# Kernel tuning notes

Hardware: AMD Instinct MI355X
Metric: run time of the kernel (lower is better)

The kernel has to match this reference:

```python
import jax, jax.numpy as jnp
import numpy as np

HIDDEN = 512
BATCH = 64
SEQ = 1024


def setup_inputs() -> dict:
    key = jax.random.key(0)
    ks = jax.random.split(key, 16)
    H = HIDDEN
    s = 0.05
    inp = {
        'x': jax.random.normal(ks[0], (BATCH, SEQ), dtype=jnp.float32),
        # layer 1: input size 1
        'W_ih1': jax.random.normal(ks[1], (4 * H, 1), dtype=jnp.float32) * s,
        'W_hh1': jax.random.normal(ks[2], (4 * H, H), dtype=jnp.float32) * s,
        'b_ih1': jax.random.normal(ks[3], (4 * H,), dtype=jnp.float32) * s,
        'b_hh1': jax.random.normal(ks[4], (4 * H,), dtype=jnp.float32) * s,
        # layer 2
        'W_ih2': jax.random.normal(ks[5], (4 * H, H), dtype=jnp.float32) * s,
        'W_hh2': jax.random.normal(ks[6], (4 * H, H), dtype=jnp.float32) * s,
        'b_ih2': jax.random.normal(ks[7], (4 * H,), dtype=jnp.float32) * s,
        'b_hh2': jax.random.normal(ks[8], (4 * H,), dtype=jnp.float32) * s,
        # layer 3
        'W_ih3': jax.random.normal(ks[9], (4 * H, H), dtype=jnp.float32) * s,
        'W_hh3': jax.random.normal(ks[10], (4 * H, H), dtype=jnp.float32) * s,
        'b_ih3': jax.random.normal(ks[11], (4 * H,), dtype=jnp.float32) * s,
        'b_hh3': jax.random.normal(ks[12], (4 * H,), dtype=jnp.float32) * s,
        # output projection
        'W_lin': jax.random.normal(ks[13], (1, H), dtype=jnp.float32) * s,
        'b_lin': jax.random.normal(ks[14], (1,), dtype=jnp.float32) * s,
    }
    return inp


def _lstm_cell(x, h, c, W_ih, W_hh, b_ih, b_hh):
    # PyTorch LSTMCell: gates ordered [i, f, g, o]
    gates = x @ W_ih.T + b_ih + h @ W_hh.T + b_hh  # [B, 4H]
    i, f, g, o = jnp.split(gates, 4, axis=-1)
    i = jax.nn.sigmoid(i)
    f = jax.nn.sigmoid(f)
    g = jnp.tanh(g)
    o = jax.nn.sigmoid(o)
    c_new = f * c + i * g
    h_new = o * jnp.tanh(c_new)
    return h_new, c_new


def reference(x, W_ih1, W_hh1, b_ih1, b_hh1,
              W_ih2, W_hh2, b_ih2, b_hh2,
              W_ih3, W_hh3, b_ih3, b_hh3,
              W_lin, b_lin):
    B = x.shape[0]
    H = W_hh1.shape[1]
    z = jnp.zeros((B, H), dtype=x.dtype)
    init = (z, z, z, z, z, z)  # h1,c1,h2,c2,h3,c3

    def step(carry, x_t):
        h1, c1, h2, c2, h3, c3 = carry
        h1, c1 = _lstm_cell(x_t, h1, c1, W_ih1, W_hh1, b_ih1, b_hh1)
        h2, c2 = _lstm_cell(h1, h2, c2, W_ih2, W_hh2, b_ih2, b_hh2)
        h3, c3 = _lstm_cell(h2, h3, c3, W_ih3, W_hh3, b_ih3, b_hh3)
        out = h3 @ W_lin.T + b_lin  # [B, 1]
        return (h1, c1, h2, c2, h3, c3), out

    xs = x.T[:, :, None]  # [T, B, 1]
    _, outs = jax.lax.scan(step, init, xs)  # outs: [T, B, 1]
    return outs[:, :, 0].T  # [B, T]
```

## Files before the change

kernel.cpp:

```cpp
#include <hip/hip_runtime.h>
#include <cstdint>
#include <cstddef>


typedef __attribute__((ext_vector_type(8))) short bf16x8;
typedef __attribute__((ext_vector_type(4))) float f32x4;
typedef __attribute__((ext_vector_type(2))) unsigned long long u64x2;

#define TT    1024
#define RINGD 8
#define NBL   64
#define NGRID (3*NBL + 1)
#define SENT  0xFFFFFFFFu

#define OFF_W1   0ULL
#define OFF_W2   (OFF_W1 + 2048ULL*512*2)
#define OFF_W3   (OFF_W2 + 2048ULL*1024*2)
#define OFF_BIAS (OFF_W3 + 2048ULL*1024*2)
#define OFF_FLAG (OFF_BIAS + 3ULL*2048*4)
#define OFF_RING (OFF_FLAG + 4096ULL)
#define NEED_BIG (OFF_RING + 3ULL*TT*64*512*2)

__device__ __forceinline__ unsigned short f2bf(float f) {
  unsigned int u = __float_as_uint(f);
  unsigned int r = (u + 0x7fffu + ((u >> 16) & 1u)) >> 16;
  return (unsigned short)r;
}
__device__ __forceinline__ float bf2f(unsigned short h) {
  return __uint_as_float(((unsigned int)h) << 16);
}
__device__ __forceinline__ float sigmf_(float z) {
  return 1.f / (1.f + __expf(-z));
}
__device__ __forceinline__ float tanhf_(float z) {
  float t = __expf(-2.f * fabsf(z));
  float r = (1.f - t) / (1.f + t);
  return (z < 0.f) ? -r : r;
}

__global__ void prep_kernel(const float* __restrict__ wih1, const float* __restrict__ whh1,
                            const float* __restrict__ bih1, const float* __restrict__ bhh1,
                            const float* __restrict__ wih2, const float* __restrict__ whh2,
                            const float* __restrict__ bih2, const float* __restrict__ bhh2,
                            const float* __restrict__ wih3, const float* __restrict__ whh3,
                            const float* __restrict__ bih3, const float* __restrict__ bhh3,
                            unsigned char* ws, int big)
{
  unsigned short* w1 = (unsigned short*)(ws + OFF_W1);
  unsigned short* w2 = (unsigned short*)(ws + OFF_W2);
  unsigned short* w3 = (unsigned short*)(ws + OFF_W3);
  float* bias = (float*)(ws + OFF_BIAS);
  int*   flags = (int*)(ws + OFF_FLAG);
  int idx = blockIdx.x * 256 + threadIdx.x;
  int j = idx >> 10, k = idx & 1023;
  if (j < 2048) {
    float v2 = (k < 512) ? wih2[j*512 + k] : whh2[j*512 + (k - 512)];
    float v3 = (k < 512) ? wih3[j*512 + k] : whh3[j*512 + (k - 512)];
    w2[j*1024 + k] = f2bf(v2);
    w3[j*1024 + k] = f2bf(v3);
    if (k < 512) w1[j*512 + k] = f2bf(whh1[j*512 + k]);
  }
  if (idx < 2048) {
    bias[idx]        = bih1[idx] + bhh1[idx];
    bias[2048 + idx] = bih2[idx] + bhh2[idx];
    bias[4096 + idx] = bih3[idx] + bhh3[idx];
  }
  if (idx < 256) flags[idx] = 0;
  if (big) {
    uint4* r4 = (uint4*)(ws + OFF_RING);
    uint4 s; s.x = SENT; s.y = SENT; s.z = SENT; s.w = SENT;
    for (size_t i = idx; i < 12582912ULL; i += 2097152ULL) r4[i] = s;
  }
}

template<int KSTEPS>
__device__ __forceinline__ void compute_tiles(const bf16x8 (&warr)[32], const char* smemc,
                                              int wv, int ln15, int kgrp,
                                              f32x4 (&acc)[2][4])
{
  const int k0w = wv * (KSTEPS * 32);
  const int sw  = (ln15 & 7) << 4;
  #pragma unroll
  for (int s = 0; s < KSTEPS; ++s) {
    const int koff = k0w + s*32 + kgrp*8;
    const int r    = koff >> 9;
    const int kin  = koff & 511;
    const char* ab = smemc + r*32768;
    bf16x8 a0 = *(const bf16x8*)(ab + ((ln15*1024        + kin*2) ^ sw));
    bf16x8 a1 = *(const bf16x8*)(ab + (((ln15 + 16)*1024 + kin*2) ^ sw));
    #pragma unroll
    for (int gt = 0; gt < 4; ++gt) {
      acc[0][gt] = __builtin_amdgcn_mfma_f32_16x16x32_bf16(a0, warr[gt*KSTEPS + s], acc[0][gt], 0, 0, 0);
      acc[1][gt] = __builtin_amdgcn_mfma_f32_16x16x32_bf16(a1, warr[gt*KSTEPS + s], acc[1][gt], 0, 0, 0);
    }
  }
}

__global__ __launch_bounds__(256, 1) void rnn_kernel(
    unsigned char* ws, const float* __restrict__ x,
    const float* __restrict__ wih1, const float* __restrict__ wlin,
    const float* __restrict__ blin, float* __restrict__ out, int big)
{
  __shared__ __align__(128) char smem[65536];
  const int tid  = threadIdx.x;
  const int lane = tid & 63;
  const int wv   = tid >> 6;
  const int SLOTS = big ? TT : RINGD;
  int* flags = (int*)(ws + OFF_FLAG);
  unsigned int* ringw = (unsigned int*)(ws + OFF_RING);
  const unsigned long long* ringq = (const unsigned long long*)(ws + OFF_RING);

  if (blockIdx.x == NGRID - 1) {
    float* wl = (float*)smem;
    float* op = (float*)(smem + 4096);
    if (tid < 128) ((f32x4*)wl)[tid] = ((const f32x4*)wlin)[tid];
    float blv = blin[0];
    __syncthreads();
    const int ob = tid >> 2, okq = tid & 3;
    const int* fup = flags + 2*64 + lane;
    for (int t = 0; t < TT; ++t) {
      if (!big && wv == 0) {
        for (;;) {
          int v = __hip_atomic_load(fup, __ATOMIC_RELAXED, __HIP_MEMORY_SCOPE_AGENT);
          if (__all(v >= t + 1)) break;
          __builtin_amdgcn_s_sleep(2);
        }
      }
      asm volatile("" ::: "memory");
      __syncthreads();
      const int slot = big ? t : (t & 7);
      size_t ebase = ((size_t)(2*SLOTS + slot) * 64 + ob) * 512 + (size_t)okq * 128;
      const unsigned long long* hp = ringq + (ebase >> 2);
      const float* wlp = wl + okq * 128;
      unsigned long long qv[32];
      if (big) {
        #pragma unroll
        for (int i = 0; i < 32; ++i) qv[i] = hp[i];
        for (;;) {
          int bad = 0;
          #pragma unroll
          for (int i = 0; i < 32; ++i)
            bad |= ((unsigned int)qv[i] == SENT) | ((unsigned int)(qv[i] >> 32) == SENT);
          if (!bad) break;
          __builtin_amdgcn_s_sleep(2);
          #pragma unroll
          for (int i = 0; i < 32; ++i)
            qv[i] = __hip_atomic_load(hp + i, __ATOMIC_RELAXED, __HIP_MEMORY_SCOPE_AGENT);
        }
      } else {
        #pragma unroll
        for (int i = 0; i < 32; ++i)
          qv[i] = __hip_atomic_load(hp + i, __ATOMIC_RELAXED, __HIP_MEMORY_SCOPE_AGENT);
      }
      float acc = 0.f;
      #pragma unroll
      for (int i = 0; i < 32; ++i) {
        acc += bf2f((unsigned short)(qv[i]      )) * wlp[i*4 + 0];
        acc += bf2f((unsigned short)(qv[i] >> 16)) * wlp[i*4 + 1];
        acc += bf2f((unsigned short)(qv[i] >> 32)) * wlp[i*4 + 2];
        acc += bf2f((unsigned short)(qv[i] >> 48)) * wlp[i*4 + 3];
      }
      op[ob*4 + okq] = acc;
      __syncthreads();
      if (tid < 64)
        out[(size_t)tid * TT + t] = op[tid*4] + op[tid*4+1] + op[tid*4+2] + op[tid*4+3] + blv;
      if (!big && tid == 0)
        __hip_atomic_store(flags + 3*64, t + 1, __ATOMIC_RELEASE, __HIP_MEMORY_SCOPE_AGENT);
      __syncthreads();
    }
    return;
  }

  const int g  = blockIdx.x >> 6;
  const int q  = blockIdx.x & 63;
  const int bh = q & 1;
  const int nbase = (q >> 1) << 4;
  const unsigned short* Wg =
      (const unsigned short*)(ws + (g == 0 ? OFF_W1 : (g == 1 ? OFF_W2 : OFF_W3)));
  const float* biasg = (const float*)(ws + OFF_BIAS) + g * 2048;

  const int ln15 = lane & 15;
  const int kgrp = lane >> 4;

  bf16x8 warr[32];
  if (g == 0) {
    #pragma unroll
    for (int gt = 0; gt < 4; ++gt)
      #pragma unroll
      for (int s = 0; s < 4; ++s)
        warr[gt*4 + s] = *(const bf16x8*)(Wg + (size_t)(gt*512 + nbase + ln15)*512
                                             + wv*128 + s*32 + kgrp*8);
  } else {
    #pragma unroll
    for (int gt = 0; gt < 4; ++gt)
      #pragma unroll
      for (int s = 0; s < 8; ++s)
        warr[gt*8 + s] = *(const bf16x8*)(Wg + (size_t)(gt*512 + nbase + ln15)*1024
                                             + wv*256 + s*32 + kgrp*8);
  }

  const int eb  = tid >> 3;
  const int n0  = (tid & 7) << 1;
  const int bge = bh * 32 + eb;
  float bsv[4][2], wxv[4][2];
  #pragma unroll
  for (int gt = 0; gt < 4; ++gt) {
    #pragma unroll
    for (int cc = 0; cc < 2; ++cc) {
      int jj = gt*512 + nbase + n0 + cc;
      bsv[gt][cc] = biasg[jj];
      wxv[gt][cc] = (g == 0) ? wih1[jj] : 0.f;
    }
  }
  float cst0 = 0.f, cst1 = 0.f;

  const int l31 = lane & 31;
  int* myflag = flags + g*64 + q;
  const int* fup  = flags + (g > 0 ? (g - 1)*64 : 0) + 2*l31 + bh;
  const int* fsib = flags + g*64 + 2*l31 + bh;
  const int* fdn  = (g < 2) ? (flags + (g + 1)*64 + 2*l31 + bh) : (flags + 3*64);

  const int sbi = tid >> 3, skc = tid & 7;
  const int swz = (sbi & 7) << 4;

  auto stage_big = [&](int gg, int tick, int r) {
    size_t ebase = ((size_t)(gg*TT + tick) * 64 + bh*32 + sbi) * 512;
    const unsigned long long* src = ringq + (ebase >> 2);
    char* dst = smem + r*32768 + sbi*1024;
    unsigned long long v[16];
    #pragma unroll
    for (int i = 0; i < 8; ++i) {
      v[2*i]   = src[(i*8 + skc)*2];
      v[2*i+1] = src[(i*8 + skc)*2 + 1];
    }
    for (;;) {
      int bad = 0;
      #pragma unroll
      for (int i = 0; i < 16; ++i)
        bad |= ((unsigned int)v[i] == SENT) | ((unsigned int)(v[i] >> 32) == SENT);
      if (!bad) break;
      __builtin_amdgcn_s_sleep(2);
      #pragma unroll
      for (int i = 0; i < 8; ++i) {
        v[2*i]   = __hip_atomic_load(src + (i*8 + skc)*2,     __ATOMIC_RELAXED, __HIP_MEMORY_SCOPE_AGENT);
        v[2*i+1] = __hip_atomic_load(src + (i*8 + skc)*2 + 1, __ATOMIC_RELAXED, __HIP_MEMORY_SCOPE_AGENT);
      }
    }
    #pragma unroll
    for (int i = 0; i < 8; ++i) {
      u64x2 w; w[0] = v[2*i]; w[1] = v[2*i+1];
      *(u64x2*)(dst + (((i*8 + skc) * 16) ^ swz)) = w;
    }
  };
  auto stage_small = [&](int gg, int slot, int r) {
    size_t ebase = ((size_t)(gg*RINGD + slot) * 64 + bh*32 + sbi) * 512;
    const unsigned long long* src = ringq + (ebase >> 2);
    char* dst = smem + r*32768 + sbi*1024;
    unsigned long long v[16];
    #pragma unroll
    for (int i = 0; i < 16; ++i)
      v[i] = __hip_atomic_load(src + (i*8 + skc), __ATOMIC_RELAXED, __HIP_MEMORY_SCOPE_AGENT);
    #pragma unroll
    for (int i = 0; i < 16; ++i)
      *(unsigned long long*)(dst + (((i*8 + skc) * 8) ^ swz)) = v[i];
  };
  auto zero_region = [&](int r) {
    char* dst = smem + r*32768 + sbi*1024;
    #pragma unroll
    for (int i = 0; i < 16; ++i)
      *(unsigned long long*)(dst + (((i*8 + skc) * 8) ^ swz)) = 0ULL;
  };

  if (g > 0) {
    if (big) {
      stage_big(g - 1, 0, 0);
    } else {
      if (wv == 0) {
        for (;;) {
          int v = __hip_atomic_load(fup, __ATOMIC_RELAXED, __HIP_MEMORY_SCOPE_AGENT);
          if (__all(v >= 1)) break;
          __builtin_amdgcn_s_sleep(2);
        }
      }
      asm volatile("" ::: "memory");
      __syncthreads();
      stage_small(g - 1, 0, 0);
    }
  }

  for (int t = 0; t < TT; ++t) {
    const int slot = big ? t : (t & 7);
    if (!big && wv == 0) {
      for (;;) {
        int ok = 1;
        if (t >= 1) {
          int v = __hip_atomic_load(fsib, __ATOMIC_RELAXED, __HIP_MEMORY_SCOPE_AGENT);
          ok &= (v >= t);
        }
        if (t >= RINGD) {
          int v = __hip_atomic_load(fdn, __ATOMIC_RELAXED, __HIP_MEMORY_SCOPE_AGENT);
          ok &= (v >= t - RINGD + 1);
        }
        if (__all(ok)) break;
        __builtin_amdgcn_s_sleep(2);
      }
    }
    asm volatile("" ::: "memory");
    __syncthreads();
    const int hr = (g == 0) ? 0 : 1;
    if (t == 0)       zero_region(hr);
    else if (big)     stage_big(g, t - 1, hr);
    else              stage_small(g, (t - 1) & 7, hr);
    __syncthreads();

    f32x4 acc[2][4];
    #pragma unroll
    for (int a = 0; a < 2; ++a) {
      #pragma unroll
      for (int b = 0; b < 4; ++b) { f32x4 z = {0.f, 0.f, 0.f, 0.f}; acc[a][b] = z; }
    }
    if (g == 0) compute_tiles<4>(warr, smem, wv, ln15, kgrp, acc);
    else        compute_tiles<8>(warr, smem, wv, ln15, kgrp, acc);
    __syncthreads();

    float* part = (float*)smem;
    #pragma unroll
    for (int bt = 0; bt < 2; ++bt) {
      #pragma unroll
      for (int gt = 0; gt < 4; ++gt) {
        #pragma unroll
        for (int rr = 0; rr < 4; ++rr) {
          int brow = bt*16 + kgrp*4 + rr;
          int jj   = gt*16 + ln15;
          part[(wv*32 + brow)*64 + (jj ^ ((brow & 3) << 4))] = acc[bt][gt][rr];
        }
      }
    }
    __syncthreads();

    float Gv[4][2];
    #pragma unroll
    for (int gt = 0; gt < 4; ++gt) {
      #pragma unroll
      for (int cc = 0; cc < 2; ++cc) {
        int jx = (gt*16 + n0 + cc) ^ ((eb & 3) << 4);
        Gv[gt][cc] = part[(0*32 + eb)*64 + jx] + part[(1*32 + eb)*64 + jx]
                   + part[(2*32 + eb)*64 + jx] + part[(3*32 + eb)*64 + jx]
                   + bsv[gt][cc];
      }
    }
    if (g == 0) {
      float xv = x[(size_t)bge * TT + t];
      #pragma unroll
      for (int gt = 0; gt < 4; ++gt) {
        Gv[gt][0] += xv * wxv[gt][0];
        Gv[gt][1] += xv * wxv[gt][1];
      }
    }
    float i0 = sigmf_(Gv[0][0]), f0 = sigmf_(Gv[1][0]), gA = tanhf_(Gv[2][0]), o0 = sigmf_(Gv[3][0]);
    float i1 = sigmf_(Gv[0][1]), f1 = sigmf_(Gv[1][1]), gB = tanhf_(Gv[2][1]), o1 = sigmf_(Gv[3][1]);
    cst0 = f0 * cst0 + i0 * gA;
    cst1 = f1 * cst1 + i1 * gB;
    float h0 = o0 * tanhf_(cst0);
    float h1 = o1 * tanhf_(cst1);
    unsigned int packed = (unsigned int)f2bf(h0) | ((unsigned int)f2bf(h1) << 16);
    size_t eidx = ((size_t)(g*SLOTS + slot) * 64 + bge) * 512 + nbase + n0;
    __hip_atomic_store(ringw + (eidx >> 1), packed, __ATOMIC_RELAXED, __HIP_MEMORY_SCOPE_AGENT);
    __syncthreads();
    if (!big && tid == 0)
      __hip_atomic_store(myflag, t + 1, __ATOMIC_RELEASE, __HIP_MEMORY_SCOPE_AGENT);

    if (g > 0 && t + 1 < TT) {
      if (big) {
        __syncthreads();
        stage_big(g - 1, t + 1, 0);
      } else {
        if (wv == 0) {
          for (;;) {
            int v = __hip_atomic_load(fup, __ATOMIC_RELAXED, __HIP_MEMORY_SCOPE_AGENT);
            if (__all(v >= t + 2)) break;
            __builtin_amdgcn_s_sleep(2);
          }
        }
        asm volatile("" ::: "memory");
        __syncthreads();
        stage_small(g - 1, (t + 1) & 7, 0);
      }
    }
    __syncthreads();
  }
}

extern "C" void kernel_launch(void* const* d_in, const int* in_sizes, int n_in,
                              void* d_out, int out_size, void* d_ws, size_t ws_size,
                              hipStream_t stream)
{
  const float* x    = (const float*)d_in[0];
  const float* wih1 = (const float*)d_in[1];
  const float* whh1 = (const float*)d_in[2];
  const float* bih1 = (const float*)d_in[3];
  const float* bhh1 = (const float*)d_in[4];
  const float* wih2 = (const float*)d_in[5];
  const float* whh2 = (const float*)d_in[6];
  const float* bih2 = (const float*)d_in[7];
  const float* bhh2 = (const float*)d_in[8];
  const float* wih3 = (const float*)d_in[9];
  const float* whh3 = (const float*)d_in[10];
  const float* bih3 = (const float*)d_in[11];
  const float* bhh3 = (const float*)d_in[12];
  const float* wlin = (const float*)d_in[13];
  const float* blin = (const float*)d_in[14];
  unsigned char* ws = (unsigned char*)d_ws;
  float* out = (float*)d_out;

  int big = (ws_size >= NEED_BIG) ? 1 : 0;

  hipLaunchKernelGGL(prep_kernel, dim3(8192), dim3(256), 0, stream,
                     wih1, whh1, bih1, bhh1, wih2, whh2, bih2, bhh2,
                     wih3, whh3, bih3, bhh3, ws, big);

  static_assert(NGRID == 193, "grid");
  void* kws = (void*)ws;  void* kx = (void*)x;  void* kw1 = (void*)wih1;
  void* kwl = (void*)wlin; void* kbl = (void*)blin; void* ko = (void*)out;
  void* args[] = { &kws, &kx, &kw1, &kwl, &kbl, &ko, &big };
  hipError_t lerr = hipLaunchCooperativeKernel((void*)rnn_kernel, dim3(NGRID),
                                               dim3(256), args, 0, stream);
  if (lerr != hipSuccess) {
    hipLaunchKernelGGL(rnn_kernel, dim3(NGRID), dim3(256), 0, stream,
                       ws, x, wih1, wlin, blin, out, big);
  }
}
```

Measured before the change: 3.617 ms.

## Overlap ring loads with MFMA compute and move partials to separate LDS region

In the big (full-history) path, the per-step loop is restructured so that both the own-layer previous h and the next-step input from the layer below are loaded from global memory before the MFMA compute. The next-step input is spin-checked and written to LDS only after compute, hiding its latency behind the matmul. The partial-sum buffer moves to a separate 32KB LDS region, so epilogue writes no longer alias the staged operands, and several barriers are dropped. This adds register pressure from holding 16 u64x2 prefetch values across the compute, and raises LDS use to 96KB.

```diff
diff --git a/kernel.cpp b/kernel.cpp
--- a/kernel.cpp
+++ b/kernel.cpp
@@ -36,6 +36,9 @@
   float t = __expf(-2.f * fabsf(z));
   float r = (1.f - t) / (1.f + t);
   return (z < 0.f) ? -r : r;
+}
+__device__ __forceinline__ int badq(unsigned long long v) {
+  return (int)(((unsigned int)v == SENT) | ((unsigned int)(v >> 32) == SENT));
 }
 
 __global__ void prep_kernel(const float* __restrict__ wih1, const float* __restrict__ whh1,
@@ -101,7 +104,7 @@
     const float* __restrict__ wih1, const float* __restrict__ wlin,
     const float* __restrict__ blin, float* __restrict__ out, int big)
 {
-  __shared__ __align__(128) char smem[65536];
+  __shared__ __align__(128) char smem[98304];
   const int tid  = threadIdx.x;
   const int lane = tid & 63;
   const int wv   = tid >> 6;
@@ -139,8 +142,7 @@
         for (;;) {
           int bad = 0;
           #pragma unroll
-          for (int i = 0; i < 32; ++i)
-            bad |= ((unsigned int)qv[i] == SENT) | ((unsigned int)(qv[i] >> 32) == SENT);
+          for (int i = 0; i < 32; ++i) bad |= badq(qv[i]);
           if (!bad) break;
           __builtin_amdgcn_s_sleep(2);
           #pragma unroll
@@ -222,108 +224,12 @@
 
   const int sbi = tid >> 3, skc = tid & 7;
   const int swz = (sbi & 7) << 4;
-
-  auto stage_big = [&](int gg, int tick, int r) {
-    size_t ebase = ((size_t)(gg*TT + tick) * 64 + bh*32 + sbi) * 512;
-    const unsigned long long* src = ringq + (ebase >> 2);
-    char* dst = smem + r*32768 + sbi*1024;
-    unsigned long long v[16];
-    #pragma unroll
-    for (int i = 0; i < 8; ++i) {
-      v[2*i]   = src[(i*8 + skc)*2];
-      v[2*i+1] = src[(i*8 + skc)*2 + 1];
-    }
-    for (;;) {
-      int bad = 0;
-      #pragma unroll
-      for (int i = 0; i < 16; ++i)
-        bad |= ((unsigned int)v[i] == SENT) | ((unsigned int)(v[i] >> 32) == SENT);
-      if (!bad) break;
-      __builtin_amdgcn_s_sleep(2);
-      #pragma unroll
-      for (int i = 0; i < 8; ++i) {
-        v[2*i]   = __hip_atomic_load(src + (i*8 + skc)*2,     __ATOMIC_RELAXED, __HIP_MEMORY_SCOPE_AGENT);
-        v[2*i+1] = __hip_atomic_load(src + (i*8 + skc)*2 + 1, __ATOMIC_RELAXED, __HIP_MEMORY_SCOPE_AGENT);
-      }
-    }
-    #pragma unroll
-    for (int i = 0; i < 8; ++i) {
-      u64x2 w; w[0] = v[2*i]; w[1] = v[2*i+1];
-      *(u64x2*)(dst + (((i*8 + skc) * 16) ^ swz)) = w;
-    }
-  };
-  auto stage_small = [&](int gg, int slot, int r) {
-    size_t ebase = ((size_t)(gg*RINGD + slot) * 64 + bh*32 + sbi) * 512;
-    const unsigned long long* src = ringq + (ebase >> 2);
-    char* dst = smem + r*32768 + sbi*1024;
-    unsigned long long v[16];
-    #pragma unroll
-    for (int i = 0; i < 16; ++i)
-      v[i] = __hip_atomic_load(src + (i*8 + skc), __ATOMIC_RELAXED, __HIP_MEMORY_SCOPE_AGENT);
-    #pragma unroll
-    for (int i = 0; i < 16; ++i)
-      *(unsigned long long*)(dst + (((i*8 + skc) * 8) ^ swz)) = v[i];
-  };
-  auto zero_region = [&](int r) {
-    char* dst = smem + r*32768 + sbi*1024;
-    #pragma unroll
-    for (int i = 0; i < 16; ++i)
-      *(unsigned long long*)(dst + (((i*8 + skc) * 8) ^ swz)) = 0ULL;
-  };
-
-  if (g > 0) {
-    if (big) {
-      stage_big(g - 1, 0, 0);
-    } else {
-      if (wv == 0) {
-        for (;;) {
-          int v = __hip_atomic_load(fup, __ATOMIC_RELAXED, __HIP_MEMORY_SCOPE_AGENT);
-          if (__all(v >= 1)) break;
-          __builtin_amdgcn_s_sleep(2);
-        }
-      }
-      asm volatile("" ::: "memory");
-      __syncthreads();
-      stage_small(g - 1, 0, 0);
-    }
-  }
-
-  for (int t = 0; t < TT; ++t) {
-    const int slot = big ? t : (t & 7);
-    if (!big && wv == 0) {
-      for (;;) {
-        int ok = 1;
-        if (t >= 1) {
-          int v = __hip_atomic_load(fsib, __ATOMIC_RELAXED, __HIP_MEMORY_SCOPE_AGENT);
-          ok &= (v >= t);
-        }
-        if (t >= RINGD) {
-          int v = __hip_atomic_load(fdn, __ATOMIC_RELAXED, __HIP_MEMORY_SCOPE_AGENT);
-          ok &= (v >= t - RINGD + 1);
-        }
-        if (__all(ok)) break;
-        __builtin_amdgcn_s_sleep(2);
-      }
-    }
-    asm volatile("" ::: "memory");
-    __syncthreads();
-    const int hr = (g == 0) ? 0 : 1;
-    if (t == 0)       zero_region(hr);
-    else if (big)     stage_big(g, t - 1, hr);
-    else              stage_small(g, (t - 1) & 7, hr);
-    __syncthreads();
-
-    f32x4 acc[2][4];
-    #pragma unroll
-    for (int a = 0; a < 2; ++a) {
-      #pragma unroll
-      for (int b = 0; b < 4; ++b) { f32x4 z = {0.f, 0.f, 0.f, 0.f}; acc[a][b] = z; }
-    }
-    if (g == 0) compute_tiles<4>(warr, smem, wv, ln15, kgrp, acc);
-    else        compute_tiles<8>(warr, smem, wv, ln15, kgrp, acc);
-    __syncthreads();
-
-    float* part = (float*)smem;
+  char* dstR0 = smem + sbi*1024;
+  char* dstR1 = smem + 32768 + sbi*1024;
+  char* dstP  = (g == 0) ? dstR0 : dstR1;
+  float* part = (float*)(smem + 65536);
+
+  auto cell_epilogue = [&](f32x4 (&acc)[2][4], int t, int slot) {
     #pragma unroll
     for (int bt = 0; bt < 2; ++bt) {
       #pragma unroll
@@ -337,7 +243,6 @@
       }
     }
     __syncthreads();
-
     float Gv[4][2];
     #pragma unroll
     for (int gt = 0; gt < 4; ++gt) {
@@ -366,26 +271,194 @@
     unsigned int packed = (unsigned int)f2bf(h0) | ((unsigned int)f2bf(h1) << 16);
     size_t eidx = ((size_t)(g*SLOTS + slot) * 64 + bge) * 512 + nbase + n0;
     __hip_atomic_store(ringw + (eidx >> 1), packed, __ATOMIC_RELAXED, __HIP_MEMORY_SCOPE_AGENT);
-    __syncthreads();
-    if (!big && tid == 0)
+  };
+
+  if (big) {
+    if (g > 0) {
+      size_t ebase = ((size_t)((g-1)*TT + 0) * 64 + bh*32 + sbi) * 512;
+      const unsigned long long* src = ringq + (ebase >> 2);
+      unsigned long long v[16];
+      #pragma unroll
+      for (int i = 0; i < 16; ++i) v[i] = src[i*8 ? 0 : 0];
+      #pragma unroll
+      for (int i = 0; i < 16; ++i) v[i] = src[(i & 7)*16 + skc*2 + (i >> 3)];
+      for (;;) {
+        int bad = 0;
+        #pragma unroll
+        for (int i = 0; i < 16; ++i) bad |= badq(v[i]);
+        if (!bad) break;
+        __builtin_amdgcn_s_sleep(2);
+        #pragma unroll
+        for (int i = 0; i < 16; ++i)
+          v[i] = __hip_atomic_load(src + (i & 7)*16 + skc*2 + (i >> 3),
+                                   __ATOMIC_RELAXED, __HIP_MEMORY_SCOPE_AGENT);
+      }
+      #pragma unroll
+      for (int j = 0; j < 8; ++j) {
+        u64x2 w; w[0] = v[j]; w[1] = v[j + 8];
+        *(u64x2*)(dstR0 + (((j*8 + skc) * 16) ^ swz)) = w;
+      }
+    }
+
+    for (int t = 0; t < TT; ++t) {
+      const int pf = (g > 0 && t + 1 < TT) ? 1 : 0;
+      u64x2 vp[8], vi[8];
+      size_t ebP = 0, ebI = 0;
+      if (t > 0) {
+        ebP = ((size_t)(g*TT + (t-1)) * 64 + bh*32 + sbi) * 512;
+        const u64x2* src = (const u64x2*)(ringq + (ebP >> 2));
+        #pragma unroll
+        for (int j = 0; j < 8; ++j) vp[j] = src[j*8 + skc];
+      }
+      if (pf) {
+        ebI = ((size_t)((g-1)*TT + (t+1)) * 64 + bh*32 + sbi) * 512;
+        const u64x2* src = (const u64x2*)(ringq + (ebI >> 2));
+        #pragma unroll
+        for (int j = 0; j < 8; ++j) vi[j] = src[j*8 + skc];
+      }
+      if (t > 0) {
+        const unsigned long long* srcq = ringq + (ebP >> 2);
+        for (;;) {
+          int bad = 0;
+          #pragma unroll
+          for (int j = 0; j < 8; ++j) { bad |= badq(vp[j][0]); bad |= badq(vp[j][1]); }
+          if (!bad) break;
+          __builtin_amdgcn_s_sleep(2);
+          #pragma unroll
+          for (int j = 0; j < 8; ++j) {
+            vp[j][0] = __hip_atomic_load(srcq + (j*8 + skc)*2,     __ATOMIC_RELAXED, __HIP_MEMORY_SCOPE_AGENT);
+            vp[j][1] = __hip_atomic_load(srcq + (j*8 + skc)*2 + 1, __ATOMIC_RELAXED, __HIP_MEMORY_SCOPE_AGENT);
+          }
+        }
+        #pragma unroll
+        for (int j = 0; j < 8; ++j)
+          *(u64x2*)(dstP + (((j*8 + skc) * 16) ^ swz)) = vp[j];
+      } else {
+        #pragma unroll
+        for (int i = 0; i < 16; ++i)
+          *(unsigned long long*)(dstP + (((i*8 + skc) * 8) ^ swz)) = 0ULL;
+      }
+      int viBad = 0;
+      if (pf) {
+        #pragma unroll
+        for (int j = 0; j < 8; ++j) { viBad |= badq(vi[j][0]); viBad |= badq(vi[j][1]); }
+      }
+      __syncthreads();
+
+      f32x4 acc[2][4];
+      #pragma unroll
+      for (int a = 0; a < 2; ++a) {
+        #pragma unroll
+        for (int b = 0; b < 4; ++b) { f32x4 z = {0.f, 0.f, 0.f, 0.f}; acc[a][b] = z; }
+      }
+      if (g == 0) compute_tiles<4>(warr, smem, wv, ln15, kgrp, acc);
+      else        compute_tiles<8>(warr, smem, wv, ln15, kgrp, acc);
+      __syncthreads();
+
+      if (pf) {
+        const unsigned long long* srcq = ringq + (ebI >> 2);
+        while (viBad) {
+          __builtin_amdgcn_s_sleep(2);
+          #pragma unroll
+          for (int j = 0; j < 8; ++j) {
+            vi[j][0] = __hip_atomic_load(srcq + (j*8 + skc)*2,     __ATOMIC_RELAXED, __HIP_MEMORY_SCOPE_AGENT);
+            vi[j][1] = __hip_atomic_load(srcq + (j*8 + skc)*2 + 1, __ATOMIC_RELAXED, __HIP_MEMORY_SCOPE_AGENT);
+          }
+          viBad = 0;
+          #pragma unroll
+          for (int j = 0; j < 8; ++j) { viBad |= badq(vi[j][0]); viBad |= badq(vi[j][1]); }
+        }
+        #pragma unroll
+        for (int j = 0; j < 8; ++j)
+          *(u64x2*)(dstR0 + (((j*8 + skc) * 16) ^ swz)) = vi[j];
+      }
+      cell_epilogue(acc, t, t);
+    }
+    return;
+  }
+
+  auto stage_small = [&](int gg, int slot, int r) {
+    size_t ebase = ((size_t)(gg*RINGD + slot) * 64 + bh*32 + sbi) * 512;
+    const unsigned long long* src = ringq + (ebase >> 2);
+    char* dst = smem + r*32768 + sbi*1024;
+    unsigned long long v[16];
+    #pragma unroll
+    for (int i = 0; i < 16; ++i)
+      v[i] = __hip_atomic_load(src + (i*8 + skc), __ATOMIC_RELAXED, __HIP_MEMORY_SCOPE_AGENT);
+    #pragma unroll
+    for (int i = 0; i < 16; ++i)
+      *(unsigned long long*)(dst + (((i*8 + skc) * 8) ^ swz)) = v[i];
+  };
+  auto zero_region = [&](int r) {
+    char* dst = smem + r*32768 + sbi*1024;
+    #pragma unroll
+    for (int i = 0; i < 16; ++i)
+      *(unsigned long long*)(dst + (((i*8 + skc) * 8) ^ swz)) = 0ULL;
+  };
+
+  if (g > 0) {
+    if (wv == 0) {
+      for (;;) {
+        int v = __hip_atomic_load(fup, __ATOMIC_RELAXED, __HIP_MEMORY_SCOPE_AGENT);
+        if (__all(v >= 1)) break;
+        __builtin_amdgcn_s_sleep(2);
+      }
+    }
+    asm volatile("" ::: "memory");
+    __syncthreads();
+    stage_small(g - 1, 0, 0);
+  }
+
+  for (int t = 0; t < TT; ++t) {
+    const int slot = t & 7;
+    if (wv == 0) {
+      for (;;) {
+        int ok = 1;
+        if (t >= 1) {
+          int v = __hip_atomic_load(fsib, __ATOMIC_RELAXED, __HIP_MEMORY_SCOPE_AGENT);
+          ok &= (v >= t);
+        }
+        if (t >= RINGD) {
+          int v = __hip_atomic_load(fdn, __ATOMIC_RELAXED, __HIP_MEMORY_SCOPE_AGENT);
+          ok &= (v >= t - RINGD + 1);
+        }
+        if (__all(ok)) break;
+        __builtin_amdgcn_s_sleep(2);
+      }
+    }
+    asm volatile("" ::: "memory");
+    __syncthreads();
+    const int hr = (g == 0) ? 0 : 1;
+    if (t == 0) zero_region(hr);
+    else        stage_small(g, (t - 1) & 7, hr);
+    __syncthreads();
+
+    f32x4 acc[2][4];
+    #pragma unroll
+    for (int a = 0; a < 2; ++a) {
+      #pragma unroll
+      for (int b = 0; b < 4; ++b) { f32x4 z = {0.f, 0.f, 0.f, 0.f}; acc[a][b] = z; }
+    }
+    if (g == 0) compute_tiles<4>(warr, smem, wv, ln15, kgrp, acc);
+    else        compute_tiles<8>(warr, smem, wv, ln15, kgrp, acc);
+    __syncthreads();
+
+    cell_epilogue(acc, t, slot);
+    __syncthreads();
+    if (tid == 0)
       __hip_atomic_store(myflag, t + 1, __ATOMIC_RELEASE, __HIP_MEMORY_SCOPE_AGENT);
 
     if (g > 0 && t + 1 < TT) {
-      if (big) {
-        __syncthreads();
-        stage_big(g - 1, t + 1, 0);
-      } else {
-        if (wv == 0) {
-          for (;;) {
-            int v = __hip_atomic_load(fup, __ATOMIC_RELAXED, __HIP_MEMORY_SCOPE_AGENT);
-            if (__all(v >= t + 2)) break;
-            __builtin_amdgcn_s_sleep(2);
-          }
-        }
-        asm volatile("" ::: "memory");
-        __syncthreads();
-        stage_small(g - 1, (t + 1) & 7, 0);
-      }
+      if (wv == 0) {
+        for (;;) {
+          int v = __hip_atomic_load(fup, __ATOMIC_RELAXED, __HIP_MEMORY_SCOPE_AGENT);
+          if (__all(v >= t + 2)) break;
+          __builtin_amdgcn_s_sleep(2);
+        }
+      }
+      asm volatile("" ::: "memory");
+      __syncthreads();
+      stage_small(g - 1, (t + 1) & 7, 0);
     }
     __syncthreads();
   }
```

Result: slower. 4.867 ms (+34.5%).

## Add XCD-local exchange buffer with tagged words for recurrent hidden-state staging

Applied to the files above, without the earlier changes.

Remaps the persistent grid to 256 blocks so that blockIdx mod 8 selects a (layer, batch-half) group, with the intent of keeping each group's blocks on the same XCD. It adds a small exchange buffer of 64-bit words, each carrying the bf16 hidden pair tagged with the timestep, so readers poll for matching tags instead of the sentinel-checked big ring. After a bounded number of spins the reader falls back to the existing ring. This costs extra writes per step, wider polling loads and idle padding blocks, and it depends on block-to-XCD placement that the code assumes but does not enforce.

```diff
diff --git a/kernel.cpp b/kernel.cpp
--- a/kernel.cpp
+++ b/kernel.cpp
@@ -9,9 +9,9 @@
 
 #define TT    1024
 #define RINGD 8
-#define NBL   64
-#define NGRID (3*NBL + 1)
+#define NGRID 256
 #define SENT  0xFFFFFFFFu
+#define SPINMAX 512
 
 #define OFF_W1   0ULL
 #define OFF_W2   (OFF_W1 + 2048ULL*512*2)
@@ -20,6 +20,9 @@
 #define OFF_FLAG (OFF_BIAS + 3ULL*2048*4)
 #define OFF_RING (OFF_FLAG + 4096ULL)
 #define NEED_BIG (OFF_RING + 3ULL*TT*64*512*2)
+#define OFF_XCH  NEED_BIG
+#define XCH_U64  (6ULL*8*32*256)
+#define NEED_BIG2 (OFF_XCH + XCH_U64*8)
 
 __device__ __forceinline__ unsigned short f2bf(float f) {
   unsigned int u = __float_as_uint(f);
@@ -36,6 +39,9 @@
   float t = __expf(-2.f * fabsf(z));
   float r = (1.f - t) / (1.f + t);
   return (z < 0.f) ? -r : r;
+}
+__device__ __forceinline__ int badq(unsigned long long v) {
+  return (int)(((unsigned int)v == SENT) | ((unsigned int)(v >> 32) == SENT));
 }
 
 __global__ void prep_kernel(const float* __restrict__ wih1, const float* __restrict__ whh1,
@@ -44,7 +50,7 @@
                             const float* __restrict__ bih2, const float* __restrict__ bhh2,
                             const float* __restrict__ wih3, const float* __restrict__ whh3,
                             const float* __restrict__ bih3, const float* __restrict__ bhh3,
-                            unsigned char* ws, int big)
+                            unsigned char* ws, int mode)
 {
   unsigned short* w1 = (unsigned short*)(ws + OFF_W1);
   unsigned short* w2 = (unsigned short*)(ws + OFF_W2);
@@ -66,10 +72,14 @@
     bias[4096 + idx] = bih3[idx] + bhh3[idx];
   }
   if (idx < 256) flags[idx] = 0;
-  if (big) {
+  if (mode >= 1) {
     uint4* r4 = (uint4*)(ws + OFF_RING);
     uint4 s; s.x = SENT; s.y = SENT; s.z = SENT; s.w = SENT;
     for (size_t i = idx; i < 12582912ULL; i += 2097152ULL) r4[i] = s;
+    if (mode == 2 && idx < (int)(XCH_U64 / 2)) {
+      uint4* e4 = (uint4*)(ws + OFF_XCH);
+      e4[idx] = s;
+    }
   }
 }
 
@@ -99,18 +109,25 @@
 __global__ __launch_bounds__(256, 1) void rnn_kernel(
     unsigned char* ws, const float* __restrict__ x,
     const float* __restrict__ wih1, const float* __restrict__ wlin,
-    const float* __restrict__ blin, float* __restrict__ out, int big)
+    const float* __restrict__ blin, float* __restrict__ out, int mode)
 {
   __shared__ __align__(128) char smem[65536];
   const int tid  = threadIdx.x;
   const int lane = tid & 63;
   const int wv   = tid >> 6;
+  const int big  = (mode >= 1);
+  const int use2 = (mode == 2);
   const int SLOTS = big ? TT : RINGD;
   int* flags = (int*)(ws + OFF_FLAG);
   unsigned int* ringw = (unsigned int*)(ws + OFF_RING);
   const unsigned long long* ringq = (const unsigned long long*)(ws + OFF_RING);
-
-  if (blockIdx.x == NGRID - 1) {
+  unsigned long long* xch = (unsigned long long*)(ws + OFF_XCH);
+
+  const int gi = blockIdx.x & 7;
+  const int kk = blockIdx.x >> 3;
+
+  if (gi >= 6) {
+    if (!(gi == 6 && kk == 0)) return;
     float* wl = (float*)smem;
     float* op = (float*)(smem + 4096);
     if (tid < 128) ((f32x4*)wl)[tid] = ((const f32x4*)wlin)[tid];
@@ -139,8 +156,7 @@
         for (;;) {
           int bad = 0;
           #pragma unroll
-          for (int i = 0; i < 32; ++i)
-            bad |= ((unsigned int)qv[i] == SENT) | ((unsigned int)(qv[i] >> 32) == SENT);
+          for (int i = 0; i < 32; ++i) bad |= badq(qv[i]);
           if (!bad) break;
           __builtin_amdgcn_s_sleep(2);
           #pragma unroll
@@ -171,10 +187,10 @@
     return;
   }
 
-  const int g  = blockIdx.x >> 6;
-  const int q  = blockIdx.x & 63;
-  const int bh = q & 1;
-  const int nbase = (q >> 1) << 4;
+  const int g  = gi >> 1;
+  const int bh = gi & 1;
+  const int nbase = kk << 4;
+  const int q  = (kk << 1) | bh;
   const unsigned short* Wg =
       (const unsigned short*)(ws + (g == 0 ? OFF_W1 : (g == 1 ? OFF_W2 : OFF_W3)));
   const float* biasg = (const float*)(ws + OFF_BIAS) + g * 2048;
@@ -236,8 +252,7 @@
     for (;;) {
       int bad = 0;
       #pragma unroll
-      for (int i = 0; i < 16; ++i)
-        bad |= ((unsigned int)v[i] == SENT) | ((unsigned int)(v[i] >> 32) == SENT);
+      for (int i = 0; i < 16; ++i) bad |= badq(v[i]);
       if (!bad) break;
       __builtin_amdgcn_s_sleep(2);
       #pragma unroll
@@ -251,6 +266,28 @@
       u64x2 w; w[0] = v[2*i]; w[1] = v[2*i+1];
       *(u64x2*)(dst + (((i*8 + skc) * 16) ^ swz)) = w;
     }
+  };
+  auto stage_xch = [&](int tp, int r) {
+    const unsigned long long* sx =
+        xch + ((size_t)(gi*8 + (tp & 7)) * 32 + sbi) * 256;
+    char* dst = smem + r*32768 + sbi*1024;
+    unsigned long long v[32];
+    int spins = 0;
+    for (;;) {
+      #pragma unroll
+      for (int i = 0; i < 32; ++i)
+        v[i] = *(const volatile unsigned long long*)(sx + i*8 + skc);
+      int ok = 1;
+      #pragma unroll
+      for (int i = 0; i < 32; ++i)
+        ok &= ((unsigned int)(v[i] >> 32) == (unsigned int)tp);
+      if (ok) break;
+      if (++spins > SPINMAX) { stage_big(g, tp, r); return; }
+      __builtin_amdgcn_s_sleep(1);
+    }
+    #pragma unroll
+    for (int i = 0; i < 32; ++i)
+      *(unsigned int*)(dst + (((i*8 + skc) * 4) ^ swz)) = (unsigned int)v[i];
   };
   auto stage_small = [&](int gg, int slot, int r) {
     size_t ebase = ((size_t)(gg*RINGD + slot) * 64 + bh*32 + sbi) * 512;
@@ -309,6 +346,7 @@
     __syncthreads();
     const int hr = (g == 0) ? 0 : 1;
     if (t == 0)       zero_region(hr);
+    else if (use2)    stage_xch(t - 1, hr);
     else if (big)     stage_big(g, t - 1, hr);
     else              stage_small(g, (t - 1) & 7, hr);
     __syncthreads();
@@ -364,6 +402,9 @@
     float h0 = o0 * tanhf_(cst0);
     float h1 = o1 * tanhf_(cst1);
     unsigned int packed = (unsigned int)f2bf(h0) | ((unsigned int)f2bf(h1) << 16);
+    if (use2)
+      xch[((size_t)(gi*8 + (t & 7)) * 32 + eb) * 256 + (nbase >> 1) + (tid & 7)] =
+          ((unsigned long long)(unsigned int)t << 32) | (unsigned long long)packed;
     size_t eidx = ((size_t)(g*SLOTS + slot) * 64 + bge) * 512 + nbase + n0;
     __hip_atomic_store(ringw + (eidx >> 1), packed, __ATOMIC_RELAXED, __HIP_MEMORY_SCOPE_AGENT);
     __syncthreads();
@@ -413,20 +454,19 @@
   unsigned char* ws = (unsigned char*)d_ws;
   float* out = (float*)d_out;
 
-  int big = (ws_size >= NEED_BIG) ? 1 : 0;
+  int mode = (ws_size >= NEED_BIG2) ? 2 : ((ws_size >= NEED_BIG) ? 1 : 0);
 
   hipLaunchKernelGGL(prep_kernel, dim3(8192), dim3(256), 0, stream,
                      wih1, whh1, bih1, bhh1, wih2, whh2, bih2, bhh2,
-                     wih3, whh3, bih3, bhh3, ws, big);
-
-  static_assert(NGRID == 193, "grid");
+                     wih3, whh3, bih3, bhh3, ws, mode);
+
   void* kws = (void*)ws;  void* kx = (void*)x;  void* kw1 = (void*)wih1;
   void* kwl = (void*)wlin; void* kbl = (void*)blin; void* ko = (void*)out;
-  void* args[] = { &kws, &kx, &kw1, &kwl, &kbl, &ko, &big };
+  void* args[] = { &kws, &kx, &kw1, &kwl, &kbl, &ko, &mode };
   hipError_t lerr = hipLaunchCooperativeKernel((void*)rnn_kernel, dim3(NGRID),
                                                dim3(256), args, 0, stream);
   if (lerr != hipSuccess) {
     hipLaunchKernelGGL(rnn_kernel, dim3(NGRID), dim3(256), 0, stream,
-                       ws, x, wih1, wlin, blin, out, big);
-  }
-}
+                       ws, x, wih1, wlin, blin, out, mode);
+  }
+}
```

Measured after the change: 8.018 ms. +121.7%, slower.

## Pack two batch-half workgroups into one 512-thread block with software half-barriers

Applied to the files above, without the earlier changes.

Each pair of workgroups that covered the two batch halves of a hidden-unit tile is merged into one 512-thread workgroup. The grid shrinks from 193 to 97 blocks, and shared memory doubles to 128KB, split per half. Block-wide __syncthreads calls in the recurrent loop become per-half spin barriers built on LDS atomic counters, so the two halves still progress independently. This halves the number of CUs in the cooperative launch, at the cost of polling-based barriers and of two halves competing for one CU's SIMDs and LDS bandwidth.

```diff
diff --git a/kernel.cpp b/kernel.cpp
--- a/kernel.cpp
+++ b/kernel.cpp
@@ -9,8 +9,7 @@
 
 #define TT    1024
 #define RINGD 8
-#define NBL   64
-#define NGRID (3*NBL + 1)
+#define NGRID 97
 #define SENT  0xFFFFFFFFu
 
 #define OFF_W1   0ULL
@@ -36,6 +35,9 @@
   float t = __expf(-2.f * fabsf(z));
   float r = (1.f - t) / (1.f + t);
   return (z < 0.f) ? -r : r;
+}
+__device__ __forceinline__ int badq(unsigned long long v) {
+  return (int)(((unsigned int)v == SENT) | ((unsigned int)(v >> 32) == SENT));
 }
 
 __global__ void prep_kernel(const float* __restrict__ wih1, const float* __restrict__ whh1,
@@ -96,15 +98,21 @@
   }
 }
 
-__global__ __launch_bounds__(256, 1) void rnn_kernel(
+__global__ __launch_bounds__(512, 1) void rnn_kernel(
     unsigned char* ws, const float* __restrict__ x,
     const float* __restrict__ wih1, const float* __restrict__ wlin,
     const float* __restrict__ blin, float* __restrict__ out, int big)
 {
-  __shared__ __align__(128) char smem[65536];
+  __shared__ __align__(128) char smem[131072 + 64];
+  unsigned int* barc = (unsigned int*)(smem + 131072);
   const int tid  = threadIdx.x;
-  const int lane = tid & 63;
-  const int wv   = tid >> 6;
+  if (tid < 2) barc[tid] = 0;
+  __syncthreads();
+
+  const int h    = tid >> 8;
+  const int lt   = tid & 255;
+  const int lane = lt & 63;
+  const int wv   = lt >> 6;
   const int SLOTS = big ? TT : RINGD;
   int* flags = (int*)(ws + OFF_FLAG);
   unsigned int* ringw = (unsigned int*)(ws + OFF_RING);
@@ -117,9 +125,9 @@
     float blv = blin[0];
     __syncthreads();
     const int ob = tid >> 2, okq = tid & 3;
-    const int* fup = flags + 2*64 + lane;
+    const int* fup = flags + 2*64 + (tid & 63);
     for (int t = 0; t < TT; ++t) {
-      if (!big && wv == 0) {
+      if (!big && tid < 64) {
         for (;;) {
           int v = __hip_atomic_load(fup, __ATOMIC_RELAXED, __HIP_MEMORY_SCOPE_AGENT);
           if (__all(v >= t + 1)) break;
@@ -128,39 +136,40 @@
       }
       asm volatile("" ::: "memory");
       __syncthreads();
-      const int slot = big ? t : (t & 7);
-      size_t ebase = ((size_t)(2*SLOTS + slot) * 64 + ob) * 512 + (size_t)okq * 128;
-      const unsigned long long* hp = ringq + (ebase >> 2);
-      const float* wlp = wl + okq * 128;
-      unsigned long long qv[32];
-      if (big) {
-        #pragma unroll
-        for (int i = 0; i < 32; ++i) qv[i] = hp[i];
-        for (;;) {
-          int bad = 0;
+      if (tid < 256) {
+        const int slot = big ? t : (t & 7);
+        size_t ebase = ((size_t)(2*SLOTS + slot) * 64 + ob) * 512 + (size_t)okq * 128;
+        const unsigned long long* hp = ringq + (ebase >> 2);
+        const float* wlp = wl + okq * 128;
+        unsigned long long qv[32];
+        if (big) {
           #pragma unroll
-          for (int i = 0; i < 32; ++i)
-            bad |= ((unsigned int)qv[i] == SENT) | ((unsigned int)(qv[i] >> 32) == SENT);
-          if (!bad) break;
-          __builtin_amdgcn_s_sleep(2);
+          for (int i = 0; i < 32; ++i) qv[i] = hp[i];
+          for (;;) {
+            int bad = 0;
+            #pragma unroll
+            for (int i = 0; i < 32; ++i) bad |= badq(qv[i]);
+            if (!bad) break;
+            __builtin_amdgcn_s_sleep(2);
+            #pragma unroll
+            for (int i = 0; i < 32; ++i)
+              qv[i] = __hip_atomic_load(hp + i, __ATOMIC_RELAXED, __HIP_MEMORY_SCOPE_AGENT);
+          }
+        } else {
           #pragma unroll
           for (int i = 0; i < 32; ++i)
             qv[i] = __hip_atomic_load(hp + i, __ATOMIC_RELAXED, __HIP_MEMORY_SCOPE_AGENT);
         }
-      } else {
+        float acc = 0.f;
         #pragma unroll
-        for (int i = 0; i < 32; ++i)
-          qv[i] = __hip_atomic_load(hp + i, __ATOMIC_RELAXED, __HIP_MEMORY_SCOPE_AGENT);
-      }
-      float acc = 0.f;
-      #pragma unroll
-      for (int i = 0; i < 32; ++i) {
-        acc += bf2f((unsigned short)(qv[i]      )) * wlp[i*4 + 0];
-        acc += bf2f((unsigned short)(qv[i] >> 16)) * wlp[i*4 + 1];
-        acc += bf2f((unsigned short)(qv[i] >> 32)) * wlp[i*4 + 2];
-        acc += bf2f((unsigned short)(qv[i] >> 48)) * wlp[i*4 + 3];
-      }
-      op[ob*4 + okq] = acc;
+        for (int i = 0; i < 32; ++i) {
+          acc += bf2f((unsigned short)(qv[i]      )) * wlp[i*4 + 0];
+          acc += bf2f((unsigned short)(qv[i] >> 16)) * wlp[i*4 + 1];
+          acc += bf2f((unsigned short)(qv[i] >> 32)) * wlp[i*4 + 2];
+          acc += bf2f((unsigned short)(qv[i] >> 48)) * wlp[i*4 + 3];
+        }
+        op[ob*4 + okq] = acc;
+      }
       __syncthreads();
       if (tid < 64)
         out[(size_t)tid * TT + t] = op[tid*4] + op[tid*4+1] + op[tid*4+2] + op[tid*4+3] + blv;
@@ -171,13 +180,30 @@
     return;
   }
 
-  const int g  = blockIdx.x >> 6;
-  const int q  = blockIdx.x & 63;
-  const int bh = q & 1;
-  const int nbase = (q >> 1) << 4;
+  const int g  = blockIdx.x >> 5;
+  const int kk = blockIdx.x & 31;
+  const int bh = h;
+  const int nbase = kk << 4;
+  const int q  = (kk << 1) | bh;
   const unsigned short* Wg =
       (const unsigned short*)(ws + (g == 0 ? OFF_W1 : (g == 1 ? OFF_W2 : OFF_W3)));
   const float* biasg = (const float*)(ws + OFF_BIAS) + g * 2048;
+  char* hbase = smem + h * 65536;
+
+  unsigned int epoch = 0;
+  unsigned int* bc = barc + h;
+  auto softbar = [&]() {
+    asm volatile("s_waitcnt vmcnt(0) lgkmcnt(0)" ::: "memory");
+    if (lane == 0)
+      __hip_atomic_fetch_add(bc, 1u, __ATOMIC_RELAXED, __HIP_MEMORY_SCOPE_WORKGROUP);
+    epoch += 1u;
+    for (;;) {
+      unsigned int v = __hip_atomic_load(bc, __ATOMIC_RELAXED, __HIP_MEMORY_SCOPE_WORKGROUP);
+      if (v >= 4u * epoch) break;
+      __builtin_amdgcn_s_sleep(1);
+    }
+    asm volatile("" ::: "memory");
+  };
 
   const int ln15 = lane & 15;
   const int kgrp = lane >> 4;
@@ -199,8 +225,8 @@
                                              + wv*256 + s*32 + kgrp*8);
   }
 
-  const int eb  = tid >> 3;
-  const int n0  = (tid & 7) << 1;
+  const int eb  = lt >> 3;
+  const int n0  = (lt & 7) << 1;
   const int bge = bh * 32 + eb;
   float bsv[4][2], wxv[4][2];
   #pragma unroll
@@ -220,13 +246,13 @@
   const int* fsib = flags + g*64 + 2*l31 + bh;
   const int* fdn  = (g < 2) ? (flags + (g + 1)*64 + 2*l31 + bh) : (flags + 3*64);
 
-  const int sbi = tid >> 3, skc = tid & 7;
+  const int sbi = lt >> 3, skc = lt & 7;
   const int swz = (sbi & 7) << 4;
 
   auto stage_big = [&](int gg, int tick, int r) {
     size_t ebase = ((size_t)(gg*TT + tick) * 64 + bh*32 + sbi) * 512;
     const unsigned long long* src = ringq + (ebase >> 2);
-    char* dst = smem + r*32768 + sbi*1024;
+    char* dst = hbase + r*32768 + sbi*1024;
     unsigned long long v[16];
     #pragma unroll
     for (int i = 0; i < 8; ++i) {
@@ -236,8 +262,7 @@
     for (;;) {
       int bad = 0;
       #pragma unroll
-      for (int i = 0; i < 16; ++i)
-        bad |= ((unsigned int)v[i] == SENT) | ((unsigned int)(v[i] >> 32) == SENT);
+      for (int i = 0; i < 16; ++i) bad |= badq(v[i]);
       if (!bad) break;
       __builtin_amdgcn_s_sleep(2);
       #pragma unroll
@@ -255,7 +280,7 @@
   auto stage_small = [&](int gg, int slot, int r) {
     size_t ebase = ((size_t)(gg*RINGD + slot) * 64 + bh*32 + sbi) * 512;
     const unsigned long long* src = ringq + (ebase >> 2);
-    char* dst = smem + r*32768 + sbi*1024;
+    char* dst = hbase + r*32768 + sbi*1024;
     unsigned long long v[16];
     #pragma unroll
     for (int i = 0; i < 16; ++i)
@@ -265,7 +290,7 @@
       *(unsigned long long*)(dst + (((i*8 + skc) * 8) ^ swz)) = v[i];
   };
   auto zero_region = [&](int r) {
-    char* dst = smem + r*32768 + sbi*1024;
+    char* dst = hbase + r*32768 + sbi*1024;
     #pragma unroll
     for (int i = 0; i < 16; ++i)
       *(unsigned long long*)(dst + (((i*8 + skc) * 8) ^ swz)) = 0ULL;
@@ -283,7 +308,7 @@
         }
       }
       asm volatile("" ::: "memory");
-      __syncthreads();
+      softbar();
       stage_small(g - 1, 0, 0);
     }
   }
@@ -306,12 +331,12 @@
       }
     }
     asm volatile("" ::: "memory");
-    __syncthreads();
+    softbar();
     const int hr = (g == 0) ? 0 : 1;
     if (t == 0)       zero_region(hr);
     else if (big)     stage_big(g, t - 1, hr);
     else              stage_small(g, (t - 1) & 7, hr);
-    __syncthreads();
+    softbar();
 
     f32x4 acc[2][4];
     #pragma unroll
@@ -319,11 +344,11 @@
       #pragma unroll
       for (int b = 0; b < 4; ++b) { f32x4 z = {0.f, 0.f, 0.f, 0.f}; acc[a][b] = z; }
     }
-    if (g == 0) compute_tiles<4>(warr, smem, wv, ln15, kgrp, acc);
-    else        compute_tiles<8>(warr, smem, wv, ln15, kgrp, acc);
-    __syncthreads();
-
-    float* part = (float*)smem;
+    if (g == 0) compute_tiles<4>(warr, hbase, wv, ln15, kgrp, acc);
+    else        compute_tiles<8>(warr, hbase, wv, ln15, kgrp, acc);
+    softbar();
+
+    float* part = (float*)hbase;
     #pragma unroll
     for (int bt = 0; bt < 2; ++bt) {
       #pragma unroll
@@ -336,7 +361,7 @@
         }
       }
     }
-    __syncthreads();
+    softbar();
 
     float Gv[4][2];
     #pragma unroll
@@ -366,13 +391,15 @@
     unsigned int packed = (unsigned int)f2bf(h0) | ((unsigned int)f2bf(h1) << 16);
     size_t eidx = ((size_t)(g*SLOTS + slot) * 64 + bge) * 512 + nbase + n0;
     __hip_atomic_store(ringw + (eidx >> 1), packed, __ATOMIC_RELAXED, __HIP_MEMORY_SCOPE_AGENT);
-    __syncthreads();
-    if (!big && tid == 0)
+    softbar();
+    if (!big && lt == 0 && h == 0)
+      __hip_atomic_store(myflag, t + 1, __ATOMIC_RELEASE, __HIP_MEMORY_SCOPE_AGENT);
+    if (!big && lt == 0 && h == 1)
       __hip_atomic_store(myflag, t + 1, __ATOMIC_RELEASE, __HIP_MEMORY_SCOPE_AGENT);
 
     if (g > 0 && t + 1 < TT) {
       if (big) {
-        __syncthreads();
+        softbar();
         stage_big(g - 1, t + 1, 0);
       } else {
         if (wv == 0) {
@@ -383,11 +410,11 @@
           }
         }
         asm volatile("" ::: "memory");
-        __syncthreads();
+        softbar();
         stage_small(g - 1, (t + 1) & 7, 0);
       }
     }
-    __syncthreads();
+    softbar();
   }
 }
 
@@ -419,14 +446,13 @@
                      wih1, whh1, bih1, bhh1, wih2, whh2, bih2, bhh2,
                      wih3, whh3, bih3, bhh3, ws, big);
 
-  static_assert(NGRID == 193, "grid");
   void* kws = (void*)ws;  void* kx = (void*)x;  void* kw1 = (void*)wih1;
   void* kwl = (void*)wlin; void* kbl = (void*)blin; void* ko = (void*)out;
   void* args[] = { &kws, &kx, &kw1, &kwl, &kbl, &ko, &big };
   hipError_t lerr = hipLaunchCooperativeKernel((void*)rnn_kernel, dim3(NGRID),
-                                               dim3(256), args, 0, stream);
+                                               dim3(512), args, 0, stream);
   if (lerr != hipSuccess) {
-    hipLaunchKernelGGL(rnn_kernel, dim3(NGRID), dim3(256), 0, stream,
+    hipLaunchKernelGGL(rnn_kernel, dim3(NGRID), dim3(512), 0, stream,
                        ws, x, wih1, wlin, blin, out, big);
   }
 }
```

Measured after the change: 6.670 ms. 84.4% more time.
